# Kernel optimization log

Hardware: AMD Instinct MI355X
Metric: run time of the kernel (lower is better)

Reference implementation:

```python
import jax, jax.numpy as jnp
import numpy as np

N_NODES = 100000
N_EDGES = 3200000
N_GRAPHS = 512
N_LAYERS = 4
D = 24  # in/out channels of every TransformerConv (mask keeps all 24 features)


def _linear_params(key, fan_in, fan_out):
    k1, k2 = jax.random.split(key)
    bound = 1.0 / np.sqrt(fan_in)
    W = jax.random.uniform(k1, (fan_in, fan_out), minval=-bound, maxval=bound, dtype=jnp.float32)
    b = jax.random.uniform(k2, (fan_out,), minval=-bound, maxval=bound, dtype=jnp.float32)
    return W, b


def setup_inputs() -> dict:
    key = jax.random.key(0)
    ks = jax.random.split(key, 32)
    x = jax.random.normal(ks[0], (N_NODES, D), dtype=jnp.float32)
    edge_index = jax.random.randint(ks[1], (2, N_EDGES), 0, N_NODES, dtype=jnp.int64)
    batch = jnp.sort(jax.random.randint(ks[2], (N_NODES,), 0, N_GRAPHS, dtype=jnp.int64))
    gf = jax.random.normal(ks[3], (N_GRAPHS, 6), dtype=jnp.float32)

    # TransformerConv params per layer: lin_query/key/value/skip, all Linear(D, D) with bias
    Wq, bq, Wk, bk, Wv, bv, Ws, bs = [], [], [], [], [], [], [], []
    for l in range(N_LAYERS):
        kk = jax.random.split(ks[4 + l], 4)
        for W_list, b_list, kw in ((Wq, bq, kk[0]), (Wk, bk, kk[1]), (Wv, bv, kk[2]), (Ws, bs, kk[3])):
            W, b = _linear_params(kw, D, D)
            W_list.append(W); b_list.append(b)
    stack = lambda xs: jnp.stack(xs, axis=0)

    gfW1, gfb1 = _linear_params(ks[10], 6, 12)
    gfW2, gfb2 = _linear_params(ks[11], 12, 12)
    W1, b1 = _linear_params(ks[12], 36, 128)
    W2, b2 = _linear_params(ks[13], 128, 128)
    W3, b3 = _linear_params(ks[14], 128, 1)

    return dict(x=x, edge_index=edge_index, batch=batch, gf=gf,
                Wq=stack(Wq), bq=stack(bq), Wk=stack(Wk), bk=stack(bk),
                Wv=stack(Wv), bv=stack(bv), Ws=stack(Ws), bs=stack(bs),
                gfW1=gfW1, gfb1=gfb1, gfW2=gfW2, gfb2=gfb2,
                W1=W1, b1=b1, W2=W2, b2=b2, W3=W3, b3=b3)


def _transformer_conv(x, src, dst, Wq, bq, Wk, bk, Wv, bv, Ws, bs):
    # PyG TransformerConv, heads=1: alpha_e = softmax_dst((q[dst].k[src])/sqrt(D));
    # out = sum_e alpha_e * v[src] (scattered to dst) + lin_skip(x)
    n = x.shape[0]
    q = x @ Wq + bq
    k = x @ Wk + bk
    v = x @ Wv + bv
    logits = jnp.sum(q[dst] * k[src], axis=-1) * (1.0 / np.sqrt(D))  # [E]
    m = jax.ops.segment_max(logits, dst, num_segments=n)  # [N]; -inf for empty dst (unused)
    e = jnp.exp(logits - m[dst])
    denom = jax.ops.segment_sum(e, dst, num_segments=n) + 1e-16
    alpha = e / denom[dst]  # [E]
    agg = jax.ops.segment_sum(alpha[:, None] * v[src], dst, num_segments=n)  # [N, D]
    return agg + (x @ Ws + bs)


def reference(x, edge_index, batch, gf, Wq, bq, Wk, bk, Wv, bv, Ws, bs,
              gfW1, gfb1, gfW2, gfb2, W1, b1, W2, b2, W3, b3):
    src, dst = edge_index[0], edge_index[1]
    h = x  # mask keeps all 24 features
    for l in range(N_LAYERS):
        h = jax.nn.relu(_transformer_conv(h, src, dst, Wq[l], bq[l], Wk[l], bk[l],
                                          Wv[l], bv[l], Ws[l], bs[l]))
    # global_mean_pool over ragged graph batch
    sums = jax.ops.segment_sum(h, batch, num_segments=N_GRAPHS)
    counts = jax.ops.segment_sum(jnp.ones((h.shape[0],), h.dtype), batch, num_segments=N_GRAPHS)
    pooled = sums / jnp.maximum(counts, 1.0)[:, None]  # [G, 24]
    g = jax.nn.relu(gf @ gfW1 + gfb1)
    g = jax.nn.relu(g @ gfW2 + gfb2)  # [G, 12]
    z = jnp.concatenate([pooled, g], axis=1)  # [G, 36]
    z = jax.nn.relu(z @ W1 + b1)
    z = jax.nn.relu(z @ W2 + b2)
    z = z @ W3 + b3
    return jnp.squeeze(z, axis=-1)  # [G]
```

## Files before the change

### kernel.cpp

```cpp
#include <hip/hip_runtime.h>
#include <hip/hip_fp16.h>
#include <math.h>

#define N_NODES  100000
#define N_EDGES  3200000
#define N_GRAPHS 512
#define DCH      24
#define NLAYERS  4

#define BINSHIFT 9
#define BINSZ    512
#define NBINS    196
#define NBINS_P  200
#define CAP      17408
#define EPB      8000
#define NB_PART  400

#define KVROW    64

__global__ __launch_bounds__(256) void lin_kernel(
    const float* __restrict__ h,
    const float* __restrict__ Wq, const float* __restrict__ bq,
    const float* __restrict__ Wk, const float* __restrict__ bk,
    const float* __restrict__ Wv, const float* __restrict__ bv,
    const float* __restrict__ Ws, const float* __restrict__ bs,
    float* __restrict__ q, __half* __restrict__ kv, float* __restrict__ skip)
{
    __shared__ float sW[4 * 576];
    __shared__ float sb[4 * 24];
    for (int i = threadIdx.x; i < 576; i += blockDim.x) {
        sW[0 * 576 + i] = Wq[i];
        sW[1 * 576 + i] = Wk[i];
        sW[2 * 576 + i] = Wv[i];
        sW[3 * 576 + i] = Ws[i];
    }
    if (threadIdx.x < 24) {
        sb[0 * 24 + threadIdx.x] = bq[threadIdx.x];
        sb[1 * 24 + threadIdx.x] = bk[threadIdx.x];
        sb[2 * 24 + threadIdx.x] = bv[threadIdx.x];
        sb[3 * 24 + threadIdx.x] = bs[threadIdx.x];
    }
    __syncthreads();

    int node = blockIdx.x * blockDim.x + threadIdx.x;
    if (node >= N_NODES) return;

    float hx[24];
    const float4* hp = (const float4*)(h + (size_t)node * DCH);
    #pragma unroll
    for (int t = 0; t < 6; t++) {
        float4 f = hp[t];
        hx[4*t] = f.x; hx[4*t+1] = f.y; hx[4*t+2] = f.z; hx[4*t+3] = f.w;
    }

    #pragma unroll
    for (int mtx = 0; mtx < 4; mtx++) {
        float o[24];
        #pragma unroll
        for (int c = 0; c < 24; c++) o[c] = sb[mtx * 24 + c];
        #pragma unroll
        for (int ci = 0; ci < 24; ci++) {
            float hv = hx[ci];
            #pragma unroll
            for (int c = 0; c < 24; c++)
                o[c] += hv * sW[mtx * 576 + ci * 24 + c];
        }
        if (mtx == 0 || mtx == 3) {
            float* dst = (mtx == 0) ? (q + (size_t)node * DCH)
                                    : (skip + (size_t)node * DCH);
            float4* op = (float4*)dst;
            #pragma unroll
            for (int t = 0; t < 6; t++) {
                float4 f;
                f.x = o[4*t]; f.y = o[4*t+1]; f.z = o[4*t+2]; f.w = o[4*t+3];
                op[t] = f;
            }
        } else {
            __half tmp[24];
            #pragma unroll
            for (int c = 0; c < 24; c++) tmp[c] = __float2half_rn(o[c]);
            float4* op = (float4*)(kv + (size_t)node * KVROW + (mtx == 1 ? 0 : 24));
            const float4* tp = (const float4*)tmp;
            #pragma unroll
            for (int t = 0; t < 3; t++) op[t] = tp[t];
        }
    }
}

__global__ void cursor_init_kernel(int* __restrict__ cursor)
{
    int t = blockIdx.x * 256 + threadIdx.x;
    if (t < NBINS) cursor[t] = t * CAP;
}

__global__ __launch_bounds__(512) void partition_kernel(
    const int* __restrict__ esrc, const int* __restrict__ edst,
    int* __restrict__ cursor, unsigned int* __restrict__ bucket)
{
    __shared__ int hist[NBINS_P];
    __shared__ int base[NBINS_P];
    for (int t = threadIdx.x; t < NBINS_P; t += 512) hist[t] = 0;
    __syncthreads();
    int e0 = blockIdx.x * EPB;
    int e1 = min(e0 + EPB, N_EDGES);
    for (int e = e0 + threadIdx.x; e < e1; e += 512)
        atomicAdd(&hist[edst[e] >> BINSHIFT], 1);
    __syncthreads();
    for (int t = threadIdx.x; t < NBINS; t += 512) {
        int hcount = hist[t];
        base[t] = hcount ? atomicAdd(&cursor[t], hcount) : 0;
    }
    __syncthreads();
    for (int t = threadIdx.x; t < NBINS_P; t += 512) hist[t] = 0;
    __syncthreads();
    for (int e = e0 + threadIdx.x; e < e1; e += 512) {
        int d = edst[e];
        int b = d >> BINSHIFT;
        int lc = atomicAdd(&hist[b], 1);
        int pos = base[b] + lc;
        if (pos < (b + 1) * CAP)
            bucket[pos] = ((unsigned)(d & (BINSZ - 1)) << 17) | (unsigned)esrc[e];
    }
}

__global__ __launch_bounds__(256) void bin_scan_kernel(
    const int* __restrict__ cursor,
    int* __restrict__ bin_base, int* __restrict__ row_start)
{
    __shared__ int sd[256];
    int t = threadIdx.x;
    int v = 0;
    if (t < NBINS) v = min(cursor[t] - t * CAP, CAP);
    sd[t] = v;
    __syncthreads();
    for (int off = 1; off < 256; off <<= 1) {
        int u = (t >= off) ? sd[t - off] : 0;
        __syncthreads();
        sd[t] += u;
        __syncthreads();
    }
    if (t < NBINS) bin_base[t] = sd[t] - v;
    if (t == 0) { bin_base[NBINS] = N_EDGES; row_start[N_NODES] = N_EDGES; }
}

__global__ __launch_bounds__(512) void bin_scatter_kernel(
    const unsigned int* __restrict__ bucket, const int* __restrict__ cursor,
    const int* __restrict__ bin_base,
    int* __restrict__ row_start, int* __restrict__ csr_src)
{
    int b = blockIdx.x;
    int node0 = b << BINSHIFT;
    int nn = min(BINSZ, N_NODES - node0);
    int ebeg = b * CAP;
    int cnt  = min(cursor[b] - b * CAP, CAP);
    int obase = bin_base[b];
    __shared__ int c0[BINSZ], s[BINSZ], cur[BINSZ];
    int tid = threadIdx.x;
    c0[tid] = 0;
    __syncthreads();
    for (int i = tid; i < cnt; i += 512)
        atomicAdd(&c0[bucket[ebeg + i] >> 17], 1);
    __syncthreads();
    s[tid] = c0[tid];
    __syncthreads();
    for (int off = 1; off < 512; off <<= 1) {
        int u = (tid >= off) ? s[tid - off] : 0;
        __syncthreads();
        s[tid] += u;
        __syncthreads();
    }
    if (tid < nn) {
        int ex = obase + s[tid] - c0[tid];
        row_start[node0 + tid] = ex;
        cur[tid] = ex;
    }
    __syncthreads();
    for (int i = tid; i < cnt; i += 512) {
        unsigned p = bucket[ebeg + i];
        int j = p >> 17;
        int pos = atomicAdd(&cur[j], 1);
        csr_src[pos] = (int)(p & 0x1FFFF);
    }
}

#define LPN 8
template<int DO_POOL>
__global__ __launch_bounds__(256) void attn_kernel(
    const float* __restrict__ q, const __half* __restrict__ kv,
    const float* __restrict__ skip,
    const int* __restrict__ row_start,
    const int* __restrict__ csr_src,
    const int* __restrict__ batch,
    float* __restrict__ out, float* __restrict__ poolc)
{
    __shared__ float spool[8][25];
    int node0 = blockIdx.x * (256 / LPN);
    if (DO_POOL) {
        for (int t = threadIdx.x; t < 8 * 25; t += 256) ((float*)spool)[t] = 0.f;
        __syncthreads();
    }

    int i   = node0 + (threadIdx.x >> 3);
    int sub = threadIdx.x & (LPN - 1);
    if (i >= N_NODES) return;

    float qr[24];
    const float4* qp = (const float4*)(q + (size_t)i * DCH);
    #pragma unroll
    for (int t = 0; t < 6; t++) {
        float4 f = qp[t];
        qr[4*t] = f.x; qr[4*t+1] = f.y; qr[4*t+2] = f.z; qr[4*t+3] = f.w;
    }

    float m = -INFINITY, s = 0.f;
    float acc[24];
    #pragma unroll
    for (int c = 0; c < 24; c++) acc[c] = 0.f;

    int beg = row_start[i];
    int end = row_start[i + 1];
    const float scale = 0.2041241452319315f;

    int src_next = (beg + sub < end) ? csr_src[beg + sub] : 0;
    for (int e = beg + sub; e < end; e += LPN) {
        int src = src_next;
        src_next = (e + LPN < end) ? csr_src[e + LPN] : 0;

        const float4* kvp = (const float4*)(kv + (size_t)src * KVROW);
        float4 kr[3], vr[3];
        #pragma unroll
        for (int t = 0; t < 3; t++) kr[t] = kvp[t];
        #pragma unroll
        for (int t = 0; t < 3; t++) vr[t] = kvp[3 + t];

        const __half2* kh = (const __half2*)kr;
        float dot = 0.f;
        #pragma unroll
        for (int j = 0; j < 12; j++) {
            float2 f = __half22float2(kh[j]);
            dot += qr[2*j] * f.x + qr[2*j+1] * f.y;
        }
        dot *= scale;

        float mn   = fmaxf(m, dot);
        float wold = __expf(m - mn);
        float w    = __expf(dot - mn);
        s = s * wold + w;
        const __half2* vh = (const __half2*)vr;
        #pragma unroll
        for (int j = 0; j < 12; j++) {
            float2 f = __half22float2(vh[j]);
            acc[2*j]   = acc[2*j]   * wold + w * f.x;
            acc[2*j+1] = acc[2*j+1] * wold + w * f.y;
        }
        m = mn;
    }

    #pragma unroll
    for (int off = 1; off < LPN; off <<= 1) {
        float m2 = __shfl_xor(m, off);
        float s2 = __shfl_xor(s, off);
        float mn = fmaxf(m, m2);
        float w1 = (m  == mn) ? 1.f : __expf(m  - mn);
        float w2 = (m2 == mn) ? 1.f : __expf(m2 - mn);
        s = s * w1 + s2 * w2;
        #pragma unroll
        for (int c = 0; c < 24; c++) {
            float a2 = __shfl_xor(acc[c], off);
            acc[c] = acc[c] * w1 + a2 * w2;
        }
        m = mn;
    }

    if (!DO_POOL) {
        if (sub == 0) {
            float inv = 1.f / (s + 1e-16f);
            const float4* sp = (const float4*)(skip + (size_t)i * DCH);
            float4* op = (float4*)(out + (size_t)i * DCH);
            #pragma unroll
            for (int t = 0; t < 6; t++) {
                float4 sk = sp[t];
                float4 r;
                r.x = fmaxf(sk.x + acc[4*t]   * inv, 0.f);
                r.y = fmaxf(sk.y + acc[4*t+1] * inv, 0.f);
                r.z = fmaxf(sk.z + acc[4*t+2] * inv, 0.f);
                r.w = fmaxf(sk.w + acc[4*t+3] * inv, 0.f);
                op[t] = r;
            }
        }
    } else {
        float inv = 1.f / (s + 1e-16f);
        const float* sp = skip + (size_t)i * DCH + 3 * sub;
        float o0 = fmaxf(sp[0] + acc[3*sub]     * inv, 0.f);
        float o1 = fmaxf(sp[1] + acc[3*sub + 1] * inv, 0.f);
        float o2 = fmaxf(sp[2] + acc[3*sub + 2] * inv, 0.f);
        int g  = batch[i];
        int g0 = batch[node0];
        int rel = g - g0;
        if (rel < 8) {
            atomicAdd(&spool[rel][3*sub],     o0);
            atomicAdd(&spool[rel][3*sub + 1], o1);
            atomicAdd(&spool[rel][3*sub + 2], o2);
            if (sub == 0) atomicAdd(&spool[rel][24], 1.f);
        } else {
            atomicAdd(&poolc[g * 25 + 3*sub],     o0);
            atomicAdd(&poolc[g * 25 + 3*sub + 1], o1);
            atomicAdd(&poolc[g * 25 + 3*sub + 2], o2);
            if (sub == 0) atomicAdd(&poolc[g * 25 + 24], 1.f);
        }
        __syncthreads();
        int g0b = batch[node0];
        for (int t = threadIdx.x; t < 8 * 25; t += 256) {
            int slot = t / 25, c = t % 25;
            float val = spool[slot][c];
            if (val != 0.f)
                atomicAdd(&poolc[(g0b + slot) * 25 + c], val);
        }
    }
}

__global__ __launch_bounds__(128) void mlp_kernel(
    const float* __restrict__ poolc,
    const float* __restrict__ gf,
    const float* __restrict__ gfW1, const float* __restrict__ gfb1,
    const float* __restrict__ gfW2, const float* __restrict__ gfb2,
    const float* __restrict__ W1, const float* __restrict__ b1,
    const float* __restrict__ W2, const float* __restrict__ b2,
    const float* __restrict__ W3, const float* __restrict__ b3,
    float* __restrict__ out)
{
    int g = blockIdx.x;
    int t = threadIdx.x;
    __shared__ float z[36];
    __shared__ float g1[12];
    __shared__ float h1[128];
    __shared__ float h2[128];
    __shared__ float wsum[2];

    if (t < 12) {
        float a = gfb1[t];
        #pragma unroll
        for (int j = 0; j < 6; j++) a += gf[g * 6 + j] * gfW1[j * 12 + t];
        g1[t] = fmaxf(a, 0.f);
    }
    if (t < 24) {
        float c = fmaxf(poolc[g * 25 + 24], 1.f);
        z[t] = poolc[g * 25 + t] / c;
    }
    __syncthreads();
    if (t < 12) {
        float a = gfb2[t];
        #pragma unroll
        for (int j = 0; j < 12; j++) a += g1[j] * gfW2[j * 12 + t];
        z[24 + t] = fmaxf(a, 0.f);
    }
    __syncthreads();
    {
        float a = b1[t];
        #pragma unroll
        for (int j = 0; j < 36; j++) a += z[j] * W1[j * 128 + t];
        h1[t] = fmaxf(a, 0.f);
    }
    __syncthreads();
    {
        float a = b2[t];
        for (int j = 0; j < 128; j++) a += h1[j] * W2[j * 128 + t];
        h2[t] = fmaxf(a, 0.f);
    }
    __syncthreads();
    float p = h2[t] * W3[t];
    for (int off = 32; off; off >>= 1) p += __shfl_down(p, off);
    if ((t & 63) == 0) wsum[t >> 6] = p;
    __syncthreads();
    if (t == 0) out[g] = wsum[0] + wsum[1] + b3[0];
}

extern "C" void kernel_launch(void* const* d_in, const int* in_sizes, int n_in,
                              void* d_out, int out_size, void* d_ws, size_t ws_size,
                              hipStream_t stream)
{
    const float* x     = (const float*)d_in[0];
    const int*   ei    = (const int*)d_in[1];
    const int*   batch = (const int*)d_in[2];
    const float* gf    = (const float*)d_in[3];
    const float* Wq    = (const float*)d_in[4];
    const float* bq    = (const float*)d_in[5];
    const float* Wk    = (const float*)d_in[6];
    const float* bk    = (const float*)d_in[7];
    const float* Wv    = (const float*)d_in[8];
    const float* bv    = (const float*)d_in[9];
    const float* Ws    = (const float*)d_in[10];
    const float* bs    = (const float*)d_in[11];
    const float* gfW1  = (const float*)d_in[12];
    const float* gfb1  = (const float*)d_in[13];
    const float* gfW2  = (const float*)d_in[14];
    const float* gfb2  = (const float*)d_in[15];
    const float* W1    = (const float*)d_in[16];
    const float* b1    = (const float*)d_in[17];
    const float* W2    = (const float*)d_in[18];
    const float* b2    = (const float*)d_in[19];
    const float* W3    = (const float*)d_in[20];
    const float* b3    = (const float*)d_in[21];
    float* out = (float*)d_out;

    const int* esrc = ei;
    const int* edst = ei + N_EDGES;

    char* ws = (char*)d_ws;
    size_t off = 0;
    auto alloc = [&](size_t bytes) -> void* {
        void* p = ws + off;
        off = (off + bytes + 255) & ~(size_t)255;
        return p;
    };
    float* q     = (float*)alloc((size_t)N_NODES * DCH * 4);
    __half* kv   = (__half*)alloc((size_t)N_NODES * KVROW * 2);
    float* hA    = (float*)alloc((size_t)N_NODES * DCH * 4);
    float* hB    = (float*)alloc((size_t)N_NODES * DCH * 4);
    float* skipb = (float*)alloc((size_t)N_NODES * DCH * 4);
    int* row_start   = (int*)alloc(((size_t)N_NODES + 1) * 4);
    int* csr_src     = (int*)alloc((size_t)N_EDGES * 4);
    unsigned int* bucket = (unsigned int*)alloc((size_t)NBINS * CAP * 4);
    int* bin_base    = (int*)alloc((size_t)(NBINS + 1) * 4);
    int* bin_cursor  = (int*)alloc((size_t)NBINS_P * 4);
    float* poolc     = (float*)alloc((size_t)N_GRAPHS * 25 * 4);

    const int NB_NODE = (N_NODES + 255) / 256;
    const int NB_ATTN = (N_NODES * LPN + 255) / 256;

    cursor_init_kernel<<<1, 256, 0, stream>>>(bin_cursor);
    partition_kernel<<<NB_PART, 512, 0, stream>>>(esrc, edst, bin_cursor, bucket);
    bin_scan_kernel<<<1, 256, 0, stream>>>(bin_cursor, bin_base, row_start);
    bin_scatter_kernel<<<NBINS, 512, 0, stream>>>(bucket, bin_cursor, bin_base, row_start, csr_src);

    hipMemsetAsync(poolc, 0, (size_t)N_GRAPHS * 25 * 4, stream);

    const float* hin = x;
    float* hbuf[2] = {hA, hB};
    for (int l = 0; l < NLAYERS; l++) {
        float* hout = (l < NLAYERS - 1) ? hbuf[l & 1] : nullptr;
        float* sk   = (l < NLAYERS - 1) ? hout : skipb;
        lin_kernel<<<NB_NODE, 256, 0, stream>>>(
            hin, Wq + l * 576, bq + l * 24, Wk + l * 576, bk + l * 24,
            Wv + l * 576, bv + l * 24, Ws + l * 576, bs + l * 24,
            q, kv, skipb);
        if (l < NLAYERS - 1) {
            attn_kernel<0><<<NB_ATTN, 256, 0, stream>>>(
                q, kv, skipb, row_start, csr_src, batch, hout, nullptr);
            hin = hout;
        } else {
            attn_kernel<1><<<NB_ATTN, 256, 0, stream>>>(
                q, kv, skipb, row_start, csr_src, batch, nullptr, poolc);
        }
    }

    mlp_kernel<<<N_GRAPHS, 128, 0, stream>>>(
        poolc, gf, gfW1, gfb1, gfW2, gfb2, W1, b1, W2, b2, W3, b3, out);
}
```

Measured before the change: 377.6 us.

## Fuse next-layer QKV/skip projection into attention kernel epilogue

Each attention kernel now ends by computing the next layer's query, key/value and skip projections from the freshly produced hidden row, using weights staged in shared memory. This removes three separate linear-kernel launches and the write and re-read of the intermediate hidden state. Buffers are double-buffered, and the second key/value buffer reuses the edge bucket scratch area. The cost is extra shared memory and register pressure in the attention kernel, plus an added block barrier.

```diff
diff --git a/kernel.cpp b/kernel.cpp
--- a/kernel.cpp
+++ b/kernel.cpp
@@ -184,25 +184,45 @@
 }
 
 #define LPN 8
-template<int DO_POOL>
-__global__ __launch_bounds__(256) void attn_kernel(
+template<int MODE>
+__global__ __launch_bounds__(256) void attn_fused(
     const float* __restrict__ q, const __half* __restrict__ kv,
     const float* __restrict__ skip,
-    const int* __restrict__ row_start,
-    const int* __restrict__ csr_src,
-    const int* __restrict__ batch,
-    float* __restrict__ out, float* __restrict__ poolc)
-{
+    const int* __restrict__ row_start, const int* __restrict__ csr_src,
+    const float* __restrict__ Wqn, const float* __restrict__ bqn,
+    const float* __restrict__ Wkn, const float* __restrict__ bkn,
+    const float* __restrict__ Wvn, const float* __restrict__ bvn,
+    const float* __restrict__ Wsn, const float* __restrict__ bsn,
+    float* __restrict__ qn, __half* __restrict__ kvn, float* __restrict__ skipn,
+    const int* __restrict__ batch, float* __restrict__ poolc)
+{
+    __shared__ float sW[4 * 576];
+    __shared__ float sb[4 * 24];
     __shared__ float spool[8][25];
-    int node0 = blockIdx.x * (256 / LPN);
-    if (DO_POOL) {
-        for (int t = threadIdx.x; t < 8 * 25; t += 256) ((float*)spool)[t] = 0.f;
-        __syncthreads();
-    }
-
-    int i   = node0 + (threadIdx.x >> 3);
-    int sub = threadIdx.x & (LPN - 1);
-    if (i >= N_NODES) return;
+
+    int tid = threadIdx.x;
+    int node0 = blockIdx.x * 32;
+
+    if (MODE == 0) {
+        for (int t = tid; t < 576; t += 256) {
+            sW[t]        = Wqn[t];
+            sW[576 + t]  = Wkn[t];
+            sW[1152 + t] = Wvn[t];
+            sW[1728 + t] = Wsn[t];
+        }
+        if (tid < 24) {
+            sb[tid]      = bqn[tid];
+            sb[24 + tid] = bkn[tid];
+            sb[48 + tid] = bvn[tid];
+            sb[72 + tid] = bsn[tid];
+        }
+    } else {
+        for (int t = tid; t < 8 * 25; t += 256) ((float*)spool)[t] = 0.f;
+        __syncthreads();
+    }
+
+    int i   = node0 + (tid >> 3);
+    int sub = tid & (LPN - 1);
 
     float qr[24];
     const float4* qp = (const float4*)(q + (size_t)i * DCH);
@@ -272,22 +292,41 @@
         m = mn;
     }
 
-    if (!DO_POOL) {
-        if (sub == 0) {
-            float inv = 1.f / (s + 1e-16f);
-            const float4* sp = (const float4*)(skip + (size_t)i * DCH);
-            float4* op = (float4*)(out + (size_t)i * DCH);
-            #pragma unroll
-            for (int t = 0; t < 6; t++) {
-                float4 sk = sp[t];
-                float4 r;
-                r.x = fmaxf(sk.x + acc[4*t]   * inv, 0.f);
-                r.y = fmaxf(sk.y + acc[4*t+1] * inv, 0.f);
-                r.z = fmaxf(sk.z + acc[4*t+2] * inv, 0.f);
-                r.w = fmaxf(sk.w + acc[4*t+3] * inv, 0.f);
-                op[t] = r;
-            }
-        }
+    if (MODE == 0) {
+        __syncthreads();
+        float inv = 1.f / (s + 1e-16f);
+        float hrow[24];
+        const float4* sp = (const float4*)(skip + (size_t)i * DCH);
+        #pragma unroll
+        for (int t = 0; t < 6; t++) {
+            float4 f = sp[t];
+            hrow[4*t]   = fmaxf(f.x + acc[4*t]   * inv, 0.f);
+            hrow[4*t+1] = fmaxf(f.y + acc[4*t+1] * inv, 0.f);
+            hrow[4*t+2] = fmaxf(f.z + acc[4*t+2] * inv, 0.f);
+            hrow[4*t+3] = fmaxf(f.w + acc[4*t+3] * inv, 0.f);
+        }
+        int c0 = 3 * sub;
+        float oq0 = sb[c0],      oq1 = sb[c0+1],      oq2 = sb[c0+2];
+        float ok0 = sb[24+c0],   ok1 = sb[24+c0+1],   ok2 = sb[24+c0+2];
+        float ov0 = sb[48+c0],   ov1 = sb[48+c0+1],   ov2 = sb[48+c0+2];
+        float os0 = sb[72+c0],   os1 = sb[72+c0+1],   os2 = sb[72+c0+2];
+        #pragma unroll
+        for (int ci = 0; ci < 24; ci++) {
+            float hv = hrow[ci];
+            const float* w = &sW[ci * 24 + c0];
+            oq0 += hv * w[0];    oq1 += hv * w[1];    oq2 += hv * w[2];
+            ok0 += hv * w[576];  ok1 += hv * w[577];  ok2 += hv * w[578];
+            ov0 += hv * w[1152]; ov1 += hv * w[1153]; ov2 += hv * w[1154];
+            os0 += hv * w[1728]; os1 += hv * w[1729]; os2 += hv * w[1730];
+        }
+        float* qo = qn + (size_t)i * DCH + c0;
+        qo[0] = oq0; qo[1] = oq1; qo[2] = oq2;
+        float* so = skipn + (size_t)i * DCH + c0;
+        so[0] = os0; so[1] = os1; so[2] = os2;
+        __half* kp = kvn + (size_t)i * KVROW + c0;
+        kp[0] = __float2half_rn(ok0); kp[1] = __float2half_rn(ok1); kp[2] = __float2half_rn(ok2);
+        __half* vp = kvn + (size_t)i * KVROW + 24 + c0;
+        vp[0] = __float2half_rn(ov0); vp[1] = __float2half_rn(ov1); vp[2] = __float2half_rn(ov2);
     } else {
         float inv = 1.f / (s + 1e-16f);
         const float* sp = skip + (size_t)i * DCH + 3 * sub;
@@ -309,12 +348,11 @@
             if (sub == 0) atomicAdd(&poolc[g * 25 + 24], 1.f);
         }
         __syncthreads();
-        int g0b = batch[node0];
-        for (int t = threadIdx.x; t < 8 * 25; t += 256) {
+        for (int t = tid; t < 8 * 25; t += 256) {
             int slot = t / 25, c = t % 25;
             float val = spool[slot][c];
             if (val != 0.f)
-                atomicAdd(&poolc[(g0b + slot) * 25 + c], val);
+                atomicAdd(&poolc[(g0 + slot) * 25 + c], val);
         }
     }
 }
@@ -413,20 +451,21 @@
         off = (off + bytes + 255) & ~(size_t)255;
         return p;
     };
-    float* q     = (float*)alloc((size_t)N_NODES * DCH * 4);
-    __half* kv   = (__half*)alloc((size_t)N_NODES * KVROW * 2);
-    float* hA    = (float*)alloc((size_t)N_NODES * DCH * 4);
-    float* hB    = (float*)alloc((size_t)N_NODES * DCH * 4);
-    float* skipb = (float*)alloc((size_t)N_NODES * DCH * 4);
+    float*  qA   = (float*)alloc((size_t)N_NODES * DCH * 4);
+    __half* kvA  = (__half*)alloc((size_t)N_NODES * KVROW * 2);
+    float*  skA  = (float*)alloc((size_t)N_NODES * DCH * 4);
+    float*  qB   = (float*)alloc((size_t)N_NODES * DCH * 4);
+    float*  skB  = (float*)alloc((size_t)N_NODES * DCH * 4);
     int* row_start   = (int*)alloc(((size_t)N_NODES + 1) * 4);
     int* csr_src     = (int*)alloc((size_t)N_EDGES * 4);
     unsigned int* bucket = (unsigned int*)alloc((size_t)NBINS * CAP * 4);
+    __half* kvB  = (__half*)bucket;
     int* bin_base    = (int*)alloc((size_t)(NBINS + 1) * 4);
     int* bin_cursor  = (int*)alloc((size_t)NBINS_P * 4);
     float* poolc     = (float*)alloc((size_t)N_GRAPHS * 25 * 4);
 
     const int NB_NODE = (N_NODES + 255) / 256;
-    const int NB_ATTN = (N_NODES * LPN + 255) / 256;
+    const int NB_ATTN = N_NODES / 32;
 
     cursor_init_kernel<<<1, 256, 0, stream>>>(bin_cursor);
     partition_kernel<<<NB_PART, 512, 0, stream>>>(esrc, edst, bin_cursor, bucket);
@@ -435,24 +474,29 @@
 
     hipMemsetAsync(poolc, 0, (size_t)N_GRAPHS * 25 * 4, stream);
 
-    const float* hin = x;
-    float* hbuf[2] = {hA, hB};
-    for (int l = 0; l < NLAYERS; l++) {
-        float* hout = (l < NLAYERS - 1) ? hbuf[l & 1] : nullptr;
-        float* sk   = (l < NLAYERS - 1) ? hout : skipb;
-        lin_kernel<<<NB_NODE, 256, 0, stream>>>(
-            hin, Wq + l * 576, bq + l * 24, Wk + l * 576, bk + l * 24,
-            Wv + l * 576, bv + l * 24, Ws + l * 576, bs + l * 24,
-            q, kv, skipb);
-        if (l < NLAYERS - 1) {
-            attn_kernel<0><<<NB_ATTN, 256, 0, stream>>>(
-                q, kv, skipb, row_start, csr_src, batch, hout, nullptr);
-            hin = hout;
-        } else {
-            attn_kernel<1><<<NB_ATTN, 256, 0, stream>>>(
-                q, kv, skipb, row_start, csr_src, batch, nullptr, poolc);
-        }
-    }
+    lin_kernel<<<NB_NODE, 256, 0, stream>>>(
+        x, Wq, bq, Wk, bk, Wv, bv, Ws, bs, qA, kvA, skA);
+
+    attn_fused<0><<<NB_ATTN, 256, 0, stream>>>(
+        qA, kvA, skA, row_start, csr_src,
+        Wq + 1*576, bq + 1*24, Wk + 1*576, bk + 1*24,
+        Wv + 1*576, bv + 1*24, Ws + 1*576, bs + 1*24,
+        qB, kvB, skB, nullptr, nullptr);
+    attn_fused<0><<<NB_ATTN, 256, 0, stream>>>(
+        qB, kvB, skB, row_start, csr_src,
+        Wq + 2*576, bq + 2*24, Wk + 2*576, bk + 2*24,
+        Wv + 2*576, bv + 2*24, Ws + 2*576, bs + 2*24,
+        qA, kvA, skA, nullptr, nullptr);
+    attn_fused<0><<<NB_ATTN, 256, 0, stream>>>(
+        qA, kvA, skA, row_start, csr_src,
+        Wq + 3*576, bq + 3*24, Wk + 3*576, bk + 3*24,
+        Wv + 3*576, bv + 3*24, Ws + 3*576, bs + 3*24,
+        qB, kvB, skB, nullptr, nullptr);
+
+    attn_fused<1><<<NB_ATTN, 256, 0, stream>>>(
+        qB, kvB, skB, row_start, csr_src,
+        nullptr, nullptr, nullptr, nullptr, nullptr, nullptr, nullptr, nullptr,
+        nullptr, nullptr, nullptr, batch, poolc);
 
     mlp_kernel<<<N_GRAPHS, 128, 0, stream>>>(
         poolc, gf, gfW1, gfb1, gfW2, gfb2, W1, b1, W2, b2, W3, b3, out);
```

After: 351.6 us. -6.9%, faster.
